# Kernel tuning notes

Hardware: AMD Instinct MI355X
Metric: run time of the kernel (lower is better)

## Reference

```python
import jax, jax.numpy as jnp
import numpy as np

B, S, D, H = 2, 2048, 2048, 16
HD = D // H
DFF = 4 * D
EPS = 1e-5


def _gelu(x):
    # tanh-approximate GELU as in the torch module
    c = jnp.sqrt(jnp.asarray(2.0 / jnp.pi, dtype=x.dtype))
    return 0.5 * x * (1.0 + jnp.tanh(c * (x + 0.044715 * x ** 3)))


def _layernorm(x, scale, shift):
    mean = jnp.mean(x, axis=-1, keepdims=True)
    var = jnp.mean((x - mean) ** 2, axis=-1, keepdims=True)  # unbiased=False
    return scale * (x - mean) / jnp.sqrt(var + EPS) + shift


def setup_inputs() -> dict:
    key = jax.random.key(0)
    ks = jax.random.split(key, 8)
    std = 0.02
    return {
        "x": jax.random.normal(ks[0], (B, S, D), dtype=jnp.float32),
        "Wq": std * jax.random.normal(ks[1], (D, D), dtype=jnp.float32),
        "Wk": std * jax.random.normal(ks[2], (D, D), dtype=jnp.float32),
        "Wv": std * jax.random.normal(ks[3], (D, D), dtype=jnp.float32),
        "Wo": std * jax.random.normal(ks[4], (D, D), dtype=jnp.float32),
        "bo": jnp.zeros((D,), dtype=jnp.float32),
        "ln1_scale": jnp.ones((D,), dtype=jnp.float32),
        "ln1_shift": jnp.zeros((D,), dtype=jnp.float32),
        "ln2_scale": jnp.ones((D,), dtype=jnp.float32),
        "ln2_shift": jnp.zeros((D,), dtype=jnp.float32),
        "W1": std * jax.random.normal(ks[5], (D, DFF), dtype=jnp.float32),
        "b1": jnp.zeros((DFF,), dtype=jnp.float32),
        "W2": std * jax.random.normal(ks[6], (DFF, D), dtype=jnp.float32),
        "b2": jnp.zeros((D,), dtype=jnp.float32),
    }


def _attention(x, Wq, Wk, Wv, Wo, bo):
    b, s, d = x.shape
    q = (x @ Wq).reshape(b, s, H, HD).transpose(0, 2, 1, 3)  # bhsd
    k = (x @ Wk).reshape(b, s, H, HD).transpose(0, 2, 1, 3)
    v = (x @ Wv).reshape(b, s, H, HD).transpose(0, 2, 1, 3)
    scores = jnp.einsum("bhqd,bhkd->bhqk", q, k)
    causal = jnp.tril(jnp.ones((s, s), dtype=bool))
    scores = jnp.where(causal, scores, -jnp.inf)
    w = jax.nn.softmax(scores / jnp.sqrt(jnp.asarray(HD, dtype=x.dtype)), axis=-1)
    ctx = jnp.einsum("bhqk,bhkd->bhqd", w, v)
    ctx = ctx.transpose(0, 2, 1, 3).reshape(b, s, d)
    return ctx @ Wo + bo


def reference(x, Wq, Wk, Wv, Wo, bo, ln1_scale, ln1_shift, ln2_scale, ln2_shift, W1, b1, W2, b2):
    # pre-LN transformer block; dropout rate 0 -> identity
    h = x + _attention(_layernorm(x, ln1_scale, ln1_shift), Wq, Wk, Wv, Wo, bo)
    y = _gelu(_layernorm(h, ln2_scale, ln2_shift) @ W1 + b1)
    return h + (y @ W2 + b2)
```

## Files before the change

### kernel.cpp

```cpp
#include <hip/hip_runtime.h>
#include <cmath>


typedef unsigned short u16;
typedef unsigned int   u32;
typedef float  f32x4  __attribute__((ext_vector_type(4)));
typedef short  s16x8  __attribute__((ext_vector_type(8)));
typedef short  s16x4  __attribute__((ext_vector_type(4)));
typedef __bf16 bf16x8 __attribute__((ext_vector_type(8)));

#define DEV __device__ __forceinline__

DEV u16 f2bf(float f) {
  union { float f; u32 u; } v; v.f = f;
  u32 u = v.u;
  u += 0x7fffu + ((u >> 16) & 1u);
  return (u16)(u >> 16);
}

DEV f32x4 mfma16(s16x8 a, s16x8 b, f32x4 c) {
  return __builtin_amdgcn_mfma_f32_16x16x32_bf16(
      __builtin_bit_cast(bf16x8, a), __builtin_bit_cast(bf16x8, b), c, 0, 0, 0);
}

DEV float gelu_f(float x) {
  const float c = 0.7978845608028654f;
  return 0.5f * x * (1.0f + tanhf(c * (x + 0.044715f * x * x * x)));
}

DEV void gload16(const u16* g, u16* l) {
  __builtin_amdgcn_global_load_lds(
      (const __attribute__((address_space(1))) u32*)(const void*)g,
      (__attribute__((address_space(3))) u32*)(void*)l, 16, 0, 0);
}

__global__ __launch_bounds__(256) void transpose_cast(
    const float* __restrict__ W, u16* __restrict__ Wt, int K, int N) {
  __shared__ float tile[32][33];
  const int n0 = blockIdx.x * 32, k0 = blockIdx.y * 32;
  const int tx = threadIdx.x, ty = threadIdx.y;
#pragma unroll
  for (int i = 0; i < 4; ++i)
    tile[ty + 8 * i][tx] = W[(size_t)(k0 + ty + 8 * i) * N + n0 + tx];
  __syncthreads();
#pragma unroll
  for (int i = 0; i < 4; ++i)
    Wt[(size_t)(n0 + ty + 8 * i) * K + k0 + tx] = f2bf(tile[tx][ty + 8 * i]);
}

__global__ __launch_bounds__(256) void ln_kernel(
    const float* __restrict__ X, const float* __restrict__ sc,
    const float* __restrict__ sh, u16* __restrict__ Y) {
  const int row = blockIdx.x, t = threadIdx.x;
  const float* xr = X + (size_t)row * 2048;
  float4 v0 = ((const float4*)xr)[t];
  float4 v1 = ((const float4*)xr)[t + 256];
  float s  = v0.x + v0.y + v0.z + v0.w + v1.x + v1.y + v1.z + v1.w;
  float qs = v0.x*v0.x + v0.y*v0.y + v0.z*v0.z + v0.w*v0.w
           + v1.x*v1.x + v1.y*v1.y + v1.z*v1.z + v1.w*v1.w;
#pragma unroll
  for (int off = 1; off < 64; off <<= 1) {
    s  += __shfl_xor(s, off);
    qs += __shfl_xor(qs, off);
  }
  __shared__ float rs[4], rq[4];
  if ((t & 63) == 0) { rs[t >> 6] = s; rq[t >> 6] = qs; }
  __syncthreads();
  const float st = rs[0] + rs[1] + rs[2] + rs[3];
  const float qt = rq[0] + rq[1] + rq[2] + rq[3];
  const float mean = st * (1.0f / 2048.0f);
  const float var  = qt * (1.0f / 2048.0f) - mean * mean;
  const float rstd = rsqrtf(var + 1e-5f);

  u16* yr = Y + (size_t)row * 2048;
  const int c0 = t * 4, c1 = 1024 + t * 4;
  s16x4 o0, o1;
  o0[0] = (short)f2bf(sc[c0+0] * (v0.x - mean) * rstd + sh[c0+0]);
  o0[1] = (short)f2bf(sc[c0+1] * (v0.y - mean) * rstd + sh[c0+1]);
  o0[2] = (short)f2bf(sc[c0+2] * (v0.z - mean) * rstd + sh[c0+2]);
  o0[3] = (short)f2bf(sc[c0+3] * (v0.w - mean) * rstd + sh[c0+3]);
  o1[0] = (short)f2bf(sc[c1+0] * (v1.x - mean) * rstd + sh[c1+0]);
  o1[1] = (short)f2bf(sc[c1+1] * (v1.y - mean) * rstd + sh[c1+1]);
  o1[2] = (short)f2bf(sc[c1+2] * (v1.z - mean) * rstd + sh[c1+2]);
  o1[3] = (short)f2bf(sc[c1+3] * (v1.w - mean) * rstd + sh[c1+3]);
  *(s16x4*)(yr + c0) = o0;
  *(s16x4*)(yr + c1) = o1;
}

template<int MHALF, int STORE_BF16, int BIAS, int RES, int GELU_ACT>
__global__ __launch_bounds__(512, 2) void gemm8(
    const u16* __restrict__ A, const u16* __restrict__ Bt,
    const float* __restrict__ bias, const float* __restrict__ res,
    float* __restrict__ Cf, u16* __restrict__ Cb,
    int M, int N, int K) {
  constexpr int NPH   = 2 * MHALF;
  constexpr int ABUFS = (MHALF == 2) ? 2 : 3;
  constexpr int ASZ   = 8192 * MHALF;
  constexpr int BOFF  = ABUFS * ASZ;
  __shared__ u16 lds[BOFF + 2 * 16384];

  const int t9 = threadIdx.x;
  const int l = t9 & 63, w = t9 >> 6;
  const int r16 = l & 15, quad = l >> 4;
  const int wm = w >> 2, wn = w & 3;

  const int nbx = N >> 8;
  const int nwg = gridDim.x;
  const int cpx = nwg >> 3;
  const int bid = blockIdx.x;
  const int swz = (bid & 7) * cpx + (bid >> 3);
  const long m0 = (long)(swz / nbx) * (128 * MHALF);
  const long n0 = (long)(swz % nbx) * 256;

  const int NT = K >> 6;
  const int srow = t9 >> 3;
  const int scol = (t9 & 7) ^ (srow & 7);

  const u16* Abase = A  + (m0 + srow) * (long)K + scol * 8;
  const u16* Bbase = Bt + (n0 + srow) * (long)K + scol * 8;
  const long rowK64  = 64 * (long)K;
  const long rowK128 = 128 * (long)K;

  #define STAGE_A(tile, h) { \
    u16* d = &lds[((tile) % ABUFS) * ASZ + (h) * 8192 + w * 512]; \
    const u16* s = Abase + (h) * rowK128 + (long)(tile) * 64; \
    gload16(s, d); gload16(s + rowK64, d + 4096); }
  #define STAGE_B(tile, h) { \
    u16* d = &lds[BOFF + ((tile) & 1) * 16384 + (h) * 8192 + w * 512]; \
    const u16* s = Bbase + (h) * rowK128 + (long)(tile) * 64; \
    gload16(s, d); gload16(s + rowK64, d + 4096); }

  f32x4 acc[4 * MHALF][4] = {};

  if (MHALF == 2) {
    STAGE_B(0, 0); STAGE_B(0, 1); STAGE_A(0, 0); STAGE_A(0, 1);
    STAGE_B(1, 0); STAGE_B(1, 1);
    asm volatile("s_waitcnt vmcnt(4)" ::: "memory");
  } else {
    STAGE_B(0, 0); STAGE_B(0, 1); STAGE_A(0, 0); STAGE_A(1, 0);
    STAGE_B(1, 0); STAGE_B(1, 1);
    asm volatile("s_waitcnt vmcnt(6)" ::: "memory");
  }
  __builtin_amdgcn_sched_barrier(0);
  __builtin_amdgcn_s_barrier();

  s16x8 bf_[4][2];
  for (int t = 0; t < NT; ++t) {
    const int ab = t % ABUFS;
    const u16* Abuf = &lds[ab * ASZ];
    const u16* Bbuf = &lds[BOFF + (t & 1) * 16384];
#pragma unroll
    for (int p = 0; p < NPH; ++p) {
      if (p == 0) {
#pragma unroll
        for (int ni = 0; ni < 4; ++ni) {
          const int brow = wn * 64 + ni * 16 + r16;
#pragma unroll
          for (int ks = 0; ks < 2; ++ks)
            bf_[ni][ks] = *(const s16x8*)&Bbuf[brow * 64 + ((ks * 4 + quad) ^ (brow & 7)) * 8];
        }
      }
      s16x8 af[2][2];
#pragma unroll
      for (int mi = 0; mi < 2; ++mi) {
        const int arow = (MHALF == 2 ? wm * 128 : wm * 64) + (2 * p + mi) * 16 + r16;
#pragma unroll
        for (int ks = 0; ks < 2; ++ks)
          af[mi][ks] = *(const s16x8*)&Abuf[arow * 64 + ((ks * 4 + quad) ^ (arow & 7)) * 8];
      }
      if (MHALF == 2) {
        if (p < 2)       { if (t + 1 < NT) STAGE_A(t + 1, p); }
        else             { if (t + 2 < NT) STAGE_B(t + 2, p - 2); }
      } else {
        if (p == 0)      { if (t + 2 < NT) STAGE_A(t + 2, 0); }
        else             { if (t + 2 < NT) { STAGE_B(t + 2, 0); STAGE_B(t + 2, 1); } }
      }
      __builtin_amdgcn_sched_barrier(0);
      __builtin_amdgcn_s_barrier();
      asm volatile("s_waitcnt lgkmcnt(0)" ::: "memory");
      __builtin_amdgcn_sched_barrier(0);
      __builtin_amdgcn_s_setprio(1);
#pragma unroll
      for (int mi = 0; mi < 2; ++mi)
#pragma unroll
        for (int ni = 0; ni < 4; ++ni)
#pragma unroll
          for (int ks = 0; ks < 2; ++ks)
            acc[2 * p + mi][ni] = mfma16(af[mi][ks], bf_[ni][ks], acc[2 * p + mi][ni]);
      __builtin_amdgcn_s_setprio(0);
      __builtin_amdgcn_sched_barrier(0);
      if (p == NPH - 1) {
        if (MHALF == 2) {
          if (t + 2 < NT) { asm volatile("s_waitcnt vmcnt(4)" ::: "memory"); }
          else            { asm volatile("s_waitcnt vmcnt(0)" ::: "memory"); }
        } else {
          if (t + 2 < NT) { asm volatile("s_waitcnt vmcnt(6)" ::: "memory"); }
          else            { asm volatile("s_waitcnt vmcnt(0)" ::: "memory"); }
        }
        __builtin_amdgcn_sched_barrier(0);
      }
      __builtin_amdgcn_s_barrier();
    }
  }
  #undef STAGE_A
  #undef STAGE_B

#pragma unroll
  for (int mi = 0; mi < 4 * MHALF; ++mi) {
#pragma unroll
    for (int ni = 0; ni < 4; ++ni) {
#pragma unroll
      for (int r = 0; r < 4; ++r) {
        const long gr = m0 + (MHALF == 2 ? wm * 128 : wm * 64) + mi * 16 + quad * 4 + r;
        const long gc = n0 + wn * 64 + ni * 16 + r16;
        float v = acc[mi][ni][r];
        if (BIAS)     v += bias[gc];
        if (GELU_ACT) v  = gelu_f(v);
        if (RES)      v += res[gr * N + gc];
        if (STORE_BF16) Cb[gr * N + gc] = f2bf(v);
        else            Cf[gr * N + gc] = v;
      }
    }
  }
}

__global__ __launch_bounds__(256) void attn_kernel(
    const u16* __restrict__ QKV, u16* __restrict__ CTX) {
  __shared__ u16 Ks[64 * 128];
  __shared__ u16 Vt[128 * 64];
  __shared__ u16 Pl[4 * 16 * 64];

  const int t = threadIdx.x;
  const int lane = t & 63, w = t >> 6;
  const int r16 = lane & 15, quad = lane >> 4;
  const int h = blockIdx.y, b = blockIdx.z;
  const long LDQ = 6144;
  const u16* Qb = QKV + (long)b * 2048 * LDQ + h * 128;
  const u16* Kb = Qb + 2048;
  const u16* Vb = Qb + 4096;
  u16* Pw = Pl + w * (16 * 64);

  const int srow = t >> 4;
  const int sslot = t & 15;
  const float scale = 0.08838834764831845f;

  for (int half = 0; half < 2; ++half) {
    const int qt = half ? (31 - (int)blockIdx.x) : (int)blockIdx.x;
    const int q0 = qt * 64;
    const int qw = q0 + w * 16;

    s16x8 aq[4];
#pragma unroll
    for (int ks = 0; ks < 4; ++ks)
      aq[ks] = *(const s16x8*)(Qb + (long)(qw + r16) * LDQ + ks * 32 + quad * 8);

    f32x4 o[8] = {};
    float mrun[4], lrun[4];
#pragma unroll
    for (int r = 0; r < 4; ++r) { mrun[r] = -1e30f; lrun[r] = 0.0f; }

    for (int kt = 0; kt <= qt; ++kt) {
      const int kbase = kt * 64;
      __syncthreads();

#pragma unroll
      for (int i = 0; i < 4; ++i) {
        const int row = i * 16 + srow;
        const int gslot = sslot ^ (row & 7);
        gload16(Kb + (long)(kbase + row) * LDQ + gslot * 8,
                Ks + i * 2048 + w * 512);
      }
      s16x8 vv[4];
#pragma unroll
      for (int i = 0; i < 4; ++i)
        vv[i] = *(const s16x8*)(Vb + (long)(kbase + i * 16 + srow) * LDQ + sslot * 8);
#pragma unroll
      for (int i = 0; i < 4; ++i) {
        const int k = i * 16 + srow;
#pragma unroll
        for (int j = 0; j < 8; ++j) {
          const int e = (j + (t & 7)) & 7;
          const int d = sslot * 8 + e;
          Vt[(d * 64 + k) ^ ((d & 7) << 3)] = (u16)vv[i][e];
        }
      }
      __syncthreads();

      f32x4 sc[4];
#pragma unroll
      for (int kh = 0; kh < 4; ++kh) {
        f32x4 z = {};
        sc[kh] = z;
        const int krow = kh * 16 + r16;
#pragma unroll
        for (int ks = 0; ks < 4; ++ks) {
          s16x8 bk = *(const s16x8*)&Ks[(krow * 128 + ks * 32 + quad * 8) ^ ((krow & 7) << 3)];
          sc[kh] = mfma16(aq[ks], bk, sc[kh]);
        }
      }

      float alpha[4];
#pragma unroll
      for (int r = 0; r < 4; ++r) {
        const int q = qw + quad * 4 + r;
        float sv[4];
#pragma unroll
        for (int kh = 0; kh < 4; ++kh) {
          float s = sc[kh][r] * scale;
          if (kbase + kh * 16 + r16 > q) s = -1e30f;
          sv[kh] = s;
        }
        float mx = fmaxf(fmaxf(sv[0], sv[1]), fmaxf(sv[2], sv[3]));
#pragma unroll
        for (int off = 1; off < 16; off <<= 1) mx = fmaxf(mx, __shfl_xor(mx, off));
        const float mn = fmaxf(mrun[r], mx);
        alpha[r] = __expf(mrun[r] - mn);
        mrun[r] = mn;
        float rsum = 0.0f;
        const int prow = quad * 4 + r;
#pragma unroll
        for (int kh = 0; kh < 4; ++kh) {
          const float p = __expf(sv[kh] - mn);
          rsum += p;
          Pw[(prow * 64 + kh * 16 + r16) ^ ((prow & 7) << 3)] = f2bf(p);
        }
#pragma unroll
        for (int off = 1; off < 16; off <<= 1) rsum += __shfl_xor(rsum, off);
        lrun[r] = lrun[r] * alpha[r] + rsum;
      }
#pragma unroll
      for (int ds = 0; ds < 8; ++ds)
#pragma unroll
        for (int r = 0; r < 4; ++r) o[ds][r] *= alpha[r];

#pragma unroll
      for (int s = 0; s < 2; ++s) {
        const s16x8 ap = *(const s16x8*)&Pw[(r16 * 64 + s * 32 + quad * 8) ^ ((r16 & 7) << 3)];
#pragma unroll
        for (int ds = 0; ds < 8; ++ds) {
          const int d = ds * 16 + r16;
          s16x8 bv = *(const s16x8*)&Vt[(d * 64 + s * 32 + quad * 8) ^ ((d & 7) << 3)];
          o[ds] = mfma16(ap, bv, o[ds]);
        }
      }
    }

#pragma unroll
    for (int ds = 0; ds < 8; ++ds)
#pragma unroll
      for (int r = 0; r < 4; ++r) {
        const float v = o[ds][r] / lrun[r];
        CTX[(long)(b * 2048 + qw + quad * 4 + r) * 2048 + h * 128 + ds * 16 + r16] = f2bf(v);
      }
  }
}

extern "C" void kernel_launch(void* const* d_in, const int* in_sizes, int n_in,
                              void* d_out, int out_size, void* d_ws, size_t ws_size,
                              hipStream_t stream) {
  (void)in_sizes; (void)n_in; (void)out_size; (void)ws_size;
  const float* x    = (const float*)d_in[0];
  const float* Wq   = (const float*)d_in[1];
  const float* Wk   = (const float*)d_in[2];
  const float* Wv   = (const float*)d_in[3];
  const float* Wo   = (const float*)d_in[4];
  const float* bo   = (const float*)d_in[5];
  const float* ln1s = (const float*)d_in[6];
  const float* ln1b = (const float*)d_in[7];
  const float* ln2s = (const float*)d_in[8];
  const float* ln2b = (const float*)d_in[9];
  const float* W1   = (const float*)d_in[10];
  const float* b1   = (const float*)d_in[11];
  const float* W2   = (const float*)d_in[12];
  const float* b2   = (const float*)d_in[13];
  float* out = (float*)d_out;

  const int Mtok = 4096, D = 2048, DFF = 8192, NQKV = 6144;

  char* w = (char*)d_ws;
  u16* Wt_qkv = (u16*)w;  w += (size_t)NQKV * D * 2;
  u16* Wt_o   = (u16*)w;  w += (size_t)D * D * 2;
  u16* Wt_1   = (u16*)w;  w += (size_t)DFF * D * 2;
  u16* Wt_2   = (u16*)w;  w += (size_t)D * DFF * 2;
  u16* Xln    = (u16*)w;  w += (size_t)Mtok * D * 2;
  u16* QKV    = (u16*)w;  w += (size_t)Mtok * NQKV * 2;
  u16* CTX    = (u16*)w;  w += (size_t)Mtok * D * 2;
  u16* Y1     = QKV;
  float* Hbuf = (float*)w; w += (size_t)Mtok * D * 4;

  const dim3 tb(32, 8, 1);
  transpose_cast<<<dim3(D / 32, D / 32), tb, 0, stream>>>(Wq, Wt_qkv,                    D, D);
  transpose_cast<<<dim3(D / 32, D / 32), tb, 0, stream>>>(Wk, Wt_qkv + (size_t)D * D,    D, D);
  transpose_cast<<<dim3(D / 32, D / 32), tb, 0, stream>>>(Wv, Wt_qkv + (size_t)2 * D * D,D, D);
  transpose_cast<<<dim3(D / 32, D / 32), tb, 0, stream>>>(Wo, Wt_o,                      D, D);
  transpose_cast<<<dim3(DFF / 32, D / 32), tb, 0, stream>>>(W1, Wt_1,                    D, DFF);
  transpose_cast<<<dim3(D / 32, DFF / 32), tb, 0, stream>>>(W2, Wt_2,                    DFF, D);

  ln_kernel<<<Mtok, 256, 0, stream>>>(x, ln1s, ln1b, Xln);

  gemm8<1, 1, 0, 0, 0><<<dim3(768), 512, 0, stream>>>(
      Xln, Wt_qkv, nullptr, nullptr, nullptr, QKV, Mtok, NQKV, D);

  attn_kernel<<<dim3(16, 16, 2), 256, 0, stream>>>(QKV, CTX);

  gemm8<1, 0, 1, 1, 0><<<dim3(256), 512, 0, stream>>>(
      CTX, Wt_o, bo, x, Hbuf, nullptr, Mtok, D, D);

  ln_kernel<<<Mtok, 256, 0, stream>>>(Hbuf, ln2s, ln2b, Xln);

  gemm8<2, 1, 1, 0, 1><<<dim3(512), 512, 0, stream>>>(
      Xln, Wt_1, b1, nullptr, nullptr, Y1, Mtok, DFF, D);

  gemm8<1, 0, 1, 1, 0><<<dim3(256), 512, 0, stream>>>(
      Y1, Wt_2, b2, Hbuf, out, nullptr, Mtok, D, DFF);
}
```

Before: 714.1 us.

## Pre-transpose V and double-buffer K/V tiles with async LDS loads in attention

Adds a separate kernel that transposes V per head into a scratch buffer, reusing the QKV weight workspace. The attention kernel can then load both K and V tiles directly into LDS with async global_load_lds, double-buffered so the next tile's load overlaps the current tile's compute. This replaces the per-element scalar LDS transpose of V. It also skips masking on fully visible tiles, skips work for waves whose rows lie entirely above the diagonal, defers the row-sum shuffle reduction to the end, and rescales O only when alpha changes. The cost is an extra kernel launch, extra memory traffic for V, and double the LDS footprint.

```diff
diff --git a/kernel.cpp b/kernel.cpp
--- a/kernel.cpp
+++ b/kernel.cpp
@@ -46,6 +46,25 @@
 #pragma unroll
   for (int i = 0; i < 4; ++i)
     Wt[(size_t)(n0 + ty + 8 * i) * K + k0 + tx] = f2bf(tile[tx][ty + 8 * i]);
+}
+
+__global__ __launch_bounds__(256) void transpose_v(
+    const u16* __restrict__ QKV, u16* __restrict__ VT) {
+  __shared__ u16 tile[32][33];
+  const int s0 = blockIdx.x * 32;
+  const int d0 = blockIdx.y * 32;
+  const int bh = blockIdx.z;
+  const int b = bh >> 4, h = bh & 15;
+  const int tx = threadIdx.x, ty = threadIdx.y;
+  const u16* src = QKV + (long)b * 2048 * 6144 + 4096 + h * 128;
+#pragma unroll
+  for (int i = 0; i < 4; ++i)
+    tile[ty + 8 * i][tx] = src[(long)(s0 + ty + 8 * i) * 6144 + d0 + tx];
+  __syncthreads();
+  u16* dst = VT + (long)bh * 128 * 2048;
+#pragma unroll
+  for (int i = 0; i < 4; ++i)
+    dst[(long)(d0 + ty + 8 * i) * 2048 + s0 + tx] = tile[tx][ty + 8 * i];
 }
 
 __global__ __launch_bounds__(256) void ln_kernel(
@@ -225,10 +244,11 @@
 }
 
 __global__ __launch_bounds__(256) void attn_kernel(
-    const u16* __restrict__ QKV, u16* __restrict__ CTX) {
-  __shared__ u16 Ks[64 * 128];
-  __shared__ u16 Vt[128 * 64];
-  __shared__ u16 Pl[4 * 16 * 64];
+    const u16* __restrict__ QKV, const u16* __restrict__ VT,
+    u16* __restrict__ CTX) {
+  __shared__ u16 Ks[2][64 * 128];
+  __shared__ u16 Vs[2][128 * 64];
+  __shared__ u16 Pl[4][16 * 64];
 
   const int t = threadIdx.x;
   const int lane = t & 63, w = t >> 6;
@@ -237,17 +257,33 @@
   const long LDQ = 6144;
   const u16* Qb = QKV + (long)b * 2048 * LDQ + h * 128;
   const u16* Kb = Qb + 2048;
-  const u16* Vb = Qb + 4096;
-  u16* Pw = Pl + w * (16 * 64);
-
-  const int srow = t >> 4;
-  const int sslot = t & 15;
+  const u16* Vtb = VT + (long)(b * 16 + h) * 128 * 2048;
+  u16* Pw = Pl[w];
   const float scale = 0.08838834764831845f;
+
+  const int k_row = t >> 4;
+  const int k_slot = t & 15;
+  const int v_row = t >> 3;
+  const int v_slot = t & 7;
+
+#define STAGE_KV(kt_, buf_)                                                    \
+  {                                                                            \
+    const int kb_ = (kt_) * 64;                                                \
+    _Pragma("unroll") for (int i = 0; i < 4; ++i) {                            \
+      const int row = i * 16 + k_row;                                          \
+      gload16(Kb + (long)(kb_ + row) * LDQ + (k_slot ^ (row & 7)) * 8,         \
+              &Ks[buf_][i * 2048 + w * 512]);                                  \
+    }                                                                          \
+    _Pragma("unroll") for (int i = 0; i < 4; ++i) {                            \
+      const int d_ = i * 32 + v_row;                                           \
+      gload16(Vtb + (long)d_ * 2048 + kb_ + (v_slot ^ (d_ & 7)) * 8,           \
+              &Vs[buf_][i * 2048 + w * 512]);                                  \
+    }                                                                          \
+  }
 
   for (int half = 0; half < 2; ++half) {
     const int qt = half ? (31 - (int)blockIdx.x) : (int)blockIdx.x;
-    const int q0 = qt * 64;
-    const int qw = q0 + w * 16;
+    const int qw = qt * 64 + w * 16;
 
     s16x8 aq[4];
 #pragma unroll
@@ -259,91 +295,86 @@
 #pragma unroll
     for (int r = 0; r < 4; ++r) { mrun[r] = -1e30f; lrun[r] = 0.0f; }
 
+    __builtin_amdgcn_s_barrier();
+    STAGE_KV(0, 0);
+    asm volatile("s_waitcnt vmcnt(0)" ::: "memory");
+    __builtin_amdgcn_s_barrier();
+
     for (int kt = 0; kt <= qt; ++kt) {
       const int kbase = kt * 64;
-      __syncthreads();
-
-#pragma unroll
-      for (int i = 0; i < 4; ++i) {
-        const int row = i * 16 + srow;
-        const int gslot = sslot ^ (row & 7);
-        gload16(Kb + (long)(kbase + row) * LDQ + gslot * 8,
-                Ks + i * 2048 + w * 512);
-      }
-      s16x8 vv[4];
-#pragma unroll
-      for (int i = 0; i < 4; ++i)
-        vv[i] = *(const s16x8*)(Vb + (long)(kbase + i * 16 + srow) * LDQ + sslot * 8);
-#pragma unroll
-      for (int i = 0; i < 4; ++i) {
-        const int k = i * 16 + srow;
-#pragma unroll
-        for (int j = 0; j < 8; ++j) {
-          const int e = (j + (t & 7)) & 7;
-          const int d = sslot * 8 + e;
-          Vt[(d * 64 + k) ^ ((d & 7) << 3)] = (u16)vv[i][e];
-        }
-      }
-      __syncthreads();
-
-      f32x4 sc[4];
-#pragma unroll
-      for (int kh = 0; kh < 4; ++kh) {
-        f32x4 z = {};
-        sc[kh] = z;
-        const int krow = kh * 16 + r16;
-#pragma unroll
-        for (int ks = 0; ks < 4; ++ks) {
-          s16x8 bk = *(const s16x8*)&Ks[(krow * 128 + ks * 32 + quad * 8) ^ ((krow & 7) << 3)];
-          sc[kh] = mfma16(aq[ks], bk, sc[kh]);
-        }
-      }
-
-      float alpha[4];
-#pragma unroll
-      for (int r = 0; r < 4; ++r) {
-        const int q = qw + quad * 4 + r;
-        float sv[4];
+      const int cur = kt & 1;
+      if (kt < qt) STAGE_KV(kt + 1, cur ^ 1);
+
+      if (kbase <= qw + 15) {
+        f32x4 sc[4];
 #pragma unroll
         for (int kh = 0; kh < 4; ++kh) {
-          float s = sc[kh][r] * scale;
-          if (kbase + kh * 16 + r16 > q) s = -1e30f;
-          sv[kh] = s;
-        }
-        float mx = fmaxf(fmaxf(sv[0], sv[1]), fmaxf(sv[2], sv[3]));
-#pragma unroll
-        for (int off = 1; off < 16; off <<= 1) mx = fmaxf(mx, __shfl_xor(mx, off));
-        const float mn = fmaxf(mrun[r], mx);
-        alpha[r] = __expf(mrun[r] - mn);
-        mrun[r] = mn;
-        float rsum = 0.0f;
-        const int prow = quad * 4 + r;
-#pragma unroll
-        for (int kh = 0; kh < 4; ++kh) {
-          const float p = __expf(sv[kh] - mn);
-          rsum += p;
-          Pw[(prow * 64 + kh * 16 + r16) ^ ((prow & 7) << 3)] = f2bf(p);
-        }
-#pragma unroll
-        for (int off = 1; off < 16; off <<= 1) rsum += __shfl_xor(rsum, off);
-        lrun[r] = lrun[r] * alpha[r] + rsum;
-      }
-#pragma unroll
-      for (int ds = 0; ds < 8; ++ds)
-#pragma unroll
-        for (int r = 0; r < 4; ++r) o[ds][r] *= alpha[r];
-
-#pragma unroll
-      for (int s = 0; s < 2; ++s) {
-        const s16x8 ap = *(const s16x8*)&Pw[(r16 * 64 + s * 32 + quad * 8) ^ ((r16 & 7) << 3)];
-#pragma unroll
-        for (int ds = 0; ds < 8; ++ds) {
-          const int d = ds * 16 + r16;
-          s16x8 bv = *(const s16x8*)&Vt[(d * 64 + s * 32 + quad * 8) ^ ((d & 7) << 3)];
-          o[ds] = mfma16(ap, bv, o[ds]);
-        }
-      }
+          f32x4 z = {};
+          sc[kh] = z;
+          const int krow = kh * 16 + r16;
+#pragma unroll
+          for (int ks = 0; ks < 4; ++ks) {
+            const s16x8 bk =
+                *(const s16x8*)&Ks[cur][krow * 128 + ((ks * 4 + quad) ^ (krow & 7)) * 8];
+            sc[kh] = mfma16(aq[ks], bk, sc[kh]);
+          }
+        }
+        const bool need_mask = (kbase + 63 > qw);
+        float alpha[4];
+#pragma unroll
+        for (int r = 0; r < 4; ++r) {
+          const int q = qw + quad * 4 + r;
+          float sv[4];
+#pragma unroll
+          for (int kh = 0; kh < 4; ++kh) {
+            float s = sc[kh][r] * scale;
+            if (need_mask && (kbase + kh * 16 + r16 > q)) s = -1e30f;
+            sv[kh] = s;
+          }
+          float mx = fmaxf(fmaxf(sv[0], sv[1]), fmaxf(sv[2], sv[3]));
+#pragma unroll
+          for (int off = 1; off < 16; off <<= 1) mx = fmaxf(mx, __shfl_xor(mx, off));
+          const float mn = fmaxf(mrun[r], mx);
+          alpha[r] = __expf(mrun[r] - mn);
+          mrun[r] = mn;
+          const int prow = quad * 4 + r;
+          float ps = 0.0f;
+#pragma unroll
+          for (int kh = 0; kh < 4; ++kh) {
+            const float p = __expf(sv[kh] - mn);
+            ps += p;
+            Pw[(prow * 64 + kh * 16 + r16) ^ ((prow & 7) << 3)] = f2bf(p);
+          }
+          lrun[r] = lrun[r] * alpha[r] + ps;
+        }
+        if (alpha[0] != 1.0f || alpha[1] != 1.0f || alpha[2] != 1.0f || alpha[3] != 1.0f) {
+#pragma unroll
+          for (int ds = 0; ds < 8; ++ds)
+#pragma unroll
+            for (int r = 0; r < 4; ++r) o[ds][r] *= alpha[r];
+        }
+#pragma unroll
+        for (int s = 0; s < 2; ++s) {
+          const s16x8 ap =
+              *(const s16x8*)&Pw[(r16 * 64 + s * 32 + quad * 8) ^ ((r16 & 7) << 3)];
+#pragma unroll
+          for (int ds = 0; ds < 8; ++ds) {
+            const int d = ds * 16 + r16;
+            const s16x8 bv =
+                *(const s16x8*)&Vs[cur][d * 64 + ((s * 4 + quad) ^ (d & 7)) * 8];
+            o[ds] = mfma16(ap, bv, o[ds]);
+          }
+        }
+      }
+
+      asm volatile("s_waitcnt vmcnt(0)" ::: "memory");
+      __builtin_amdgcn_s_barrier();
     }
+
+#pragma unroll
+    for (int r = 0; r < 4; ++r)
+#pragma unroll
+      for (int off = 1; off < 16; off <<= 1) lrun[r] += __shfl_xor(lrun[r], off);
 
 #pragma unroll
     for (int ds = 0; ds < 8; ++ds)
@@ -353,6 +384,7 @@
         CTX[(long)(b * 2048 + qw + quad * 4 + r) * 2048 + h * 128 + ds * 16 + r16] = f2bf(v);
       }
   }
+#undef STAGE_KV
 }
 
 extern "C" void kernel_launch(void* const* d_in, const int* in_sizes, int n_in,
@@ -386,6 +418,7 @@
   u16* QKV    = (u16*)w;  w += (size_t)Mtok * NQKV * 2;
   u16* CTX    = (u16*)w;  w += (size_t)Mtok * D * 2;
   u16* Y1     = QKV;
+  u16* VTb    = Wt_qkv;
   float* Hbuf = (float*)w; w += (size_t)Mtok * D * 4;
 
   const dim3 tb(32, 8, 1);
@@ -401,7 +434,9 @@
   gemm8<1, 1, 0, 0, 0><<<dim3(768), 512, 0, stream>>>(
       Xln, Wt_qkv, nullptr, nullptr, nullptr, QKV, Mtok, NQKV, D);
 
-  attn_kernel<<<dim3(16, 16, 2), 256, 0, stream>>>(QKV, CTX);
+  transpose_v<<<dim3(64, 4, 32), tb, 0, stream>>>(QKV, VTb);
+
+  attn_kernel<<<dim3(16, 16, 2), 256, 0, stream>>>(QKV, VTb, CTX);
 
   gemm8<1, 0, 1, 1, 0><<<dim3(256), 512, 0, stream>>>(
       CTX, Wt_o, bo, x, Hbuf, nullptr, Mtok, D, D);
```

New measurement: 643.9 us. 1.11x faster.
